# Kernel tuning notes

Measured on AMD Instinct MI355X. Metric: run time of the kernel, lower is better.

Reference implementation:

```python
import jax, jax.numpy as jnp
import numpy as np

INPUT_DIM = 1024
HIDDEN_DIM = 1024

def setup_inputs() -> dict:
    key = jax.random.key(0)
    ks = jax.random.split(key, 9)
    s_in = 1.0 / np.sqrt(INPUT_DIM)
    s_h = 1.0 / np.sqrt(HIDDEN_DIM)
    x = jax.random.normal(ks[0], (4, 2048, INPUT_DIM), dtype=jnp.float32)
    Wq = jax.random.uniform(ks[1], (INPUT_DIM, HIDDEN_DIM), jnp.float32, -s_in, s_in)
    bq = jax.random.uniform(ks[2], (HIDDEN_DIM,), jnp.float32, -s_in, s_in)
    Wk = jax.random.uniform(ks[3], (INPUT_DIM, HIDDEN_DIM), jnp.float32, -s_in, s_in)
    bk = jax.random.uniform(ks[4], (HIDDEN_DIM,), jnp.float32, -s_in, s_in)
    Wv = jax.random.uniform(ks[5], (INPUT_DIM, HIDDEN_DIM), jnp.float32, -s_in, s_in)
    bv = jax.random.uniform(ks[6], (HIDDEN_DIM,), jnp.float32, -s_in, s_in)
    Wo = jax.random.uniform(ks[7], (HIDDEN_DIM, INPUT_DIM), jnp.float32, -s_h, s_h)
    bo = jax.random.uniform(ks[8], (INPUT_DIM,), jnp.float32, -s_h, s_h)
    return {"x": x, "Wq": Wq, "bq": bq, "Wk": Wk, "bk": bk, "Wv": Wv, "bv": bv, "Wo": Wo, "bo": bo}

def reference(x, Wq, bq, Wk, bk, Wv, bv, Wo, bo):
    # x: [B, S, D_in]; scale uses x.shape[-1] (faithful to source, which divides by sqrt(input_dim))
    scale = 1.0 / jnp.sqrt(jnp.asarray(x.shape[-1], dtype=x.dtype))
    Q = jnp.einsum('bsd,dh->bsh', x, Wq) + bq
    K = jnp.einsum('bsd,dh->bsh', x, Wk) + bk
    V = jnp.einsum('bsd,dh->bsh', x, Wv) + bv
    scores = jnp.einsum('bqh,bkh->bqk', Q, K) * scale  # [B, S, S]
    attn = jax.nn.softmax(scores, axis=-1)
    ctx = jnp.einsum('bqk,bkh->bqh', attn, V)
    return jnp.einsum('bsh,hd->bsd', ctx, Wo) + bo
```

## Files before the change

kernel.cpp:

```cpp
#include <hip/hip_runtime.h>

typedef __attribute__((ext_vector_type(8))) short bf16x8;
typedef __attribute__((ext_vector_type(4))) float f32x4;
typedef __attribute__((ext_vector_type(4))) unsigned short us4;

#define AS1 __attribute__((address_space(1)))
#define AS3 __attribute__((address_space(3)))

__device__ __forceinline__ unsigned short f2bf(float f) {
  unsigned u = __float_as_uint(f);
  u += 0x7fff + ((u >> 16) & 1);
  return (unsigned short)(u >> 16);
}

__device__ __forceinline__ void gload_lds16(const void* g, void* l) {
  __builtin_amdgcn_global_load_lds((const AS1 unsigned int*)g,
                                   (AS3 unsigned int*)l, 16, 0, 0);
}

#define MFMA16(a, b, c) __builtin_amdgcn_mfma_f32_16x16x32_bf16(a, b, c, 0, 0, 0)

template <typename OutT, bool BIAS, int MODE>
__global__ __launch_bounds__(512, 2) void gemmk(
    const unsigned short* __restrict__ A,
    const unsigned short* __restrict__ Bt,
    OutT* __restrict__ C,
    unsigned short* __restrict__ Vt,
    const float* __restrict__ bias,
    int Kd, int lda, int ldb, int ldc,
    long sA, long sB, long sC,
    float scale) {
  constexpr int ABUF  = 256 * 32;
  constexpr int BUFSZ = ABUF + 128 * 32;
  __shared__ unsigned short lds[3 * BUFSZ];

  const int bz = blockIdx.z;
  A  += (size_t)bz * sA + (size_t)blockIdx.x * 256 * lda;
  Bt += (size_t)bz * sB + (size_t)blockIdx.y * 128 * ldb;

  const int tid  = threadIdx.x;
  const int wave = tid >> 6;
  const int lane = tid & 63;
  const int wm   = wave >> 1;
  const int wn   = wave & 1;
  const int l15  = lane & 15;
  const int hi   = lane >> 4;
  const int srow = tid >> 2;
  const int schk = (tid & 3) * 8;

  auto stage = [&](int bi, int k0) {
    unsigned short* L = &lds[bi * BUFSZ + wave * 512];
    const unsigned short* ga = A + (size_t)srow * lda + (k0 + schk);
    gload_lds16(ga, L);
    gload_lds16(ga + (size_t)128 * lda, L + 4096);
    gload_lds16(Bt + (size_t)srow * ldb + (k0 + schk), L + 8192);
  };

  f32x4 acc[4][4] = {};

  stage(0, 0);
  stage(1, 32);
  asm volatile("s_waitcnt vmcnt(3)" ::: "memory");
  __builtin_amdgcn_s_barrier();

  const int NT = Kd >> 5;
  int bufi = 0;
  const int rdA = (wm * 64 + l15) * 32 + hi * 8;
  const int rdB = ABUF + (wn * 64 + l15) * 32 + hi * 8;
  for (int t = 0; t < NT; ++t) {
    if (t + 2 < NT) {
      int nbi = bufi + 2; if (nbi >= 3) nbi -= 3;
      stage(nbi, (t + 2) << 5);
    }
    const unsigned short* L = &lds[bufi * BUFSZ];
    bf16x8 af[4], bf[4];
#pragma unroll
    for (int mt = 0; mt < 4; ++mt)
      af[mt] = *(const bf16x8*)&L[rdA + mt * 16 * 32];
#pragma unroll
    for (int nt = 0; nt < 4; ++nt)
      bf[nt] = *(const bf16x8*)&L[rdB + nt * 16 * 32];
    __builtin_amdgcn_s_setprio(1);
#pragma unroll
    for (int mt = 0; mt < 4; ++mt)
#pragma unroll
      for (int nt = 0; nt < 4; ++nt)
        acc[mt][nt] = MFMA16(af[mt], bf[nt], acc[mt][nt]);
    __builtin_amdgcn_s_setprio(0);
    if (t + 2 < NT)      asm volatile("s_waitcnt vmcnt(3)" ::: "memory");
    else if (t + 1 < NT) asm volatile("s_waitcnt vmcnt(0)" ::: "memory");
    __builtin_amdgcn_s_barrier();
    bufi = (bufi + 1 == 3) ? 0 : bufi + 1;
  }

  const int hi4  = hi << 2;
  const int row0 = blockIdx.x * 256 + wm * 64;
  const int col0 = blockIdx.y * 128 + wn * 64;

  if constexpr (MODE == 1) {
    const int piece = col0 >> 10;
    float bvv[4];
#pragma unroll
    for (int nt = 0; nt < 4; ++nt)
      bvv[nt] = BIAS ? bias[col0 + nt * 16 + l15] : 0.0f;
    if (piece < 2) {
      OutT* dst = C + (size_t)piece * sC;
      const int cb = (col0 & 1023) + l15;
#pragma unroll
      for (int mt = 0; mt < 4; ++mt)
#pragma unroll
        for (int r = 0; r < 4; ++r) {
          const size_t rowoff = (size_t)(row0 + mt * 16 + hi4 + r) * ldc;
#pragma unroll
          for (int nt = 0; nt < 4; ++nt)
            dst[rowoff + cb + nt * 16] = (OutT)f2bf(acc[mt][nt][r] * scale + bvv[nt]);
        }
    } else {
      const int b = blockIdx.x >> 3;
      const int sb = (blockIdx.x & 7) * 256 + wm * 64 + hi4;
#pragma unroll
      for (int nt = 0; nt < 4; ++nt) {
        const int d = ((col0 + nt * 16) & 1023) + l15;
#pragma unroll
        for (int mt = 0; mt < 4; ++mt) {
          us4 pk;
          pk.x = f2bf(acc[mt][nt][0] * scale + bvv[nt]);
          pk.y = f2bf(acc[mt][nt][1] * scale + bvv[nt]);
          pk.z = f2bf(acc[mt][nt][2] * scale + bvv[nt]);
          pk.w = f2bf(acc[mt][nt][3] * scale + bvv[nt]);
          *(us4*)&Vt[((size_t)b << 21) + (size_t)d * 2048 + sb + mt * 16] = pk;
        }
      }
    }
  } else {
    C += (size_t)bz * sC;
    float bvv[4];
#pragma unroll
    for (int nt = 0; nt < 4; ++nt)
      bvv[nt] = BIAS ? bias[col0 + nt * 16 + l15] : 0.0f;
    const int cb = col0 + l15;
#pragma unroll
    for (int mt = 0; mt < 4; ++mt)
#pragma unroll
      for (int r = 0; r < 4; ++r) {
        const size_t rowoff = (size_t)(row0 + mt * 16 + hi4 + r) * ldc;
#pragma unroll
        for (int nt = 0; nt < 4; ++nt) {
          const float v = acc[mt][nt][r] * scale + bvv[nt];
          if constexpr (sizeof(OutT) == 4)
            C[rowoff + cb + nt * 16] = v;
          else
            C[rowoff + cb + nt * 16] = (OutT)f2bf(v);
        }
      }
  }
}

__global__ void cvt_x(const float* __restrict__ in, unsigned short* __restrict__ out, int n4) {
  const int i = blockIdx.x * blockDim.x + threadIdx.x;
  if (i < n4) {
    const float4 v = ((const float4*)in)[i];
    uint2 o;
    o.x = (unsigned)f2bf(v.x) | ((unsigned)f2bf(v.y) << 16);
    o.y = (unsigned)f2bf(v.z) | ((unsigned)f2bf(v.w) << 16);
    ((uint2*)out)[i] = o;
  }
}

__global__ void cvtT_w4(const float* __restrict__ Wq, const float* __restrict__ Wk,
                        const float* __restrict__ Wv, const float* __restrict__ Wo,
                        unsigned short* __restrict__ Wqkvb, unsigned short* __restrict__ Wob) {
  __shared__ unsigned short tile[64][65];
  const int z = blockIdx.z;
  const float* in = (z == 0) ? Wq : (z == 1) ? Wk : (z == 2) ? Wv : Wo;
  unsigned short* out = (z == 3) ? Wob : Wqkvb + (size_t)z * 1024 * 1024;
  const int r0 = blockIdx.y * 64, c0 = blockIdx.x * 64;
  for (int i = threadIdx.y; i < 64; i += 4)
    tile[i][threadIdx.x] = f2bf(in[(size_t)(r0 + i) * 1024 + c0 + threadIdx.x]);
  __syncthreads();
  for (int i = threadIdx.y; i < 64; i += 4)
    out[(size_t)(c0 + i) * 1024 + r0 + threadIdx.x] = tile[threadIdx.x][i];
}

__global__ void concat_bias(const float* __restrict__ bq, const float* __restrict__ bk,
                            const float* __restrict__ bv, float* __restrict__ dst) {
  const int z = blockIdx.x;
  const float* src = (z == 0) ? bq : (z == 1) ? bk : bv;
  const int i = threadIdx.x;
  ((float4*)(dst + z * 1024))[i] = ((const float4*)src)[i];
}

__global__ __launch_bounds__(256) void softmax_bf16(unsigned short* __restrict__ scores) {
  unsigned short* p = scores + (size_t)blockIdx.x * 2048;
  const int t = threadIdx.x;
  uint4 raw = ((const uint4*)p)[t];
  float v[8];
  v[0] = __uint_as_float(raw.x << 16); v[1] = __uint_as_float(raw.x & 0xffff0000u);
  v[2] = __uint_as_float(raw.y << 16); v[3] = __uint_as_float(raw.y & 0xffff0000u);
  v[4] = __uint_as_float(raw.z << 16); v[5] = __uint_as_float(raw.z & 0xffff0000u);
  v[6] = __uint_as_float(raw.w << 16); v[7] = __uint_as_float(raw.w & 0xffff0000u);

  float m = v[0];
#pragma unroll
  for (int i = 1; i < 8; ++i) m = fmaxf(m, v[i]);
#pragma unroll
  for (int off = 32; off; off >>= 1) m = fmaxf(m, __shfl_xor(m, off, 64));

  __shared__ float red[4];
  __shared__ float bcast[2];
  const int wave = t >> 6, lane = t & 63;
  if (lane == 0) red[wave] = m;
  __syncthreads();
  if (t == 0) bcast[0] = fmaxf(fmaxf(red[0], red[1]), fmaxf(red[2], red[3]));
  __syncthreads();
  m = bcast[0];

  float s = 0.f;
#pragma unroll
  for (int i = 0; i < 8; ++i) { v[i] = __expf(v[i] - m); s += v[i]; }
#pragma unroll
  for (int off = 32; off; off >>= 1) s += __shfl_xor(s, off, 64);
  if (lane == 0) red[wave] = s;
  __syncthreads();
  if (t == 0) bcast[1] = red[0] + red[1] + red[2] + red[3];
  __syncthreads();
  const float inv = 1.0f / bcast[1];

  uint4 ov;
  ov.x = (unsigned)f2bf(v[0] * inv) | ((unsigned)f2bf(v[1] * inv) << 16);
  ov.y = (unsigned)f2bf(v[2] * inv) | ((unsigned)f2bf(v[3] * inv) << 16);
  ov.z = (unsigned)f2bf(v[4] * inv) | ((unsigned)f2bf(v[5] * inv) << 16);
  ov.w = (unsigned)f2bf(v[6] * inv) | ((unsigned)f2bf(v[7] * inv) << 16);
  ((uint4*)p)[t] = ov;
}

extern "C" void kernel_launch(void* const* d_in, const int* in_sizes, int n_in,
                              void* d_out, int out_size, void* d_ws, size_t ws_size,
                              hipStream_t stream) {
  const float* x  = (const float*)d_in[0];
  const float* Wq = (const float*)d_in[1];
  const float* bq = (const float*)d_in[2];
  const float* Wk = (const float*)d_in[3];
  const float* bk = (const float*)d_in[4];
  const float* Wv = (const float*)d_in[5];
  const float* bv = (const float*)d_in[6];
  const float* Wo = (const float*)d_in[7];
  const float* bo = (const float*)d_in[8];
  float* out = (float*)d_out;

  char* ws = (char*)d_ws;
  size_t off = 0;
  auto alloc = [&](size_t bytes) { char* p = ws + off; off += (bytes + 255) & ~255UL; return p; };
  unsigned short* xb    = (unsigned short*)alloc(8192UL * 1024 * 2);
  unsigned short* Wqkvb = (unsigned short*)alloc(3072UL * 1024 * 2);
  unsigned short* Wob   = (unsigned short*)alloc(1024UL * 1024 * 2);
  float*          bqkv  = (float*)alloc(3072UL * 4);
  unsigned short* Qb    = (unsigned short*)alloc(8192UL * 1024 * 2);
  unsigned short* Kb    = (unsigned short*)alloc(8192UL * 1024 * 2);
  unsigned short* Vtb   = (unsigned short*)alloc(4UL * 1024 * 2048 * 2);
  unsigned short* attn  = (unsigned short*)alloc(8192UL * 2048 * 2);
  unsigned short* ctxb  = (unsigned short*)alloc(8192UL * 1024 * 2);

  const dim3 blk(512);

  cvt_x<<<2097152 / 256, 256, 0, stream>>>(x, xb, 2097152);
  cvtT_w4<<<dim3(16, 16, 4), dim3(64, 4), 0, stream>>>(Wq, Wk, Wv, Wo, Wqkvb, Wob);
  concat_bias<<<3, 256, 0, stream>>>(bq, bk, bv, bqkv);

  gemmk<unsigned short, true, 1><<<dim3(32, 24, 1), blk, 0, stream>>>(
      xb, Wqkvb, Qb, Vtb, bqkv, 1024, 1024, 1024, 1024, 0, 0, 8192L * 1024, 1.0f);

  gemmk<unsigned short, false, 0><<<dim3(8, 16, 4), blk, 0, stream>>>(
      Qb, Kb, attn, nullptr, nullptr, 1024, 1024, 1024, 2048,
      2048L * 1024, 2048L * 1024, 2048L * 2048, 0.03125f);

  softmax_bf16<<<8192, 256, 0, stream>>>(attn);

  gemmk<unsigned short, false, 0><<<dim3(8, 8, 4), blk, 0, stream>>>(
      attn, Vtb, ctxb, nullptr, nullptr, 2048, 2048, 2048, 1024,
      2048L * 2048, 1024L * 2048, 2048L * 1024, 1.0f);

  gemmk<float, true, 0><<<dim3(32, 8, 1), blk, 0, stream>>>(
      ctxb, Wob, out, nullptr, bo, 1024, 1024, 1024, 1024, 0, 0, 0, 1.0f);
}
```

Before: 298.2 us.

## Template GEMM on N-tile width and use 256-wide tiles for QKV and scores

Makes the block N-tile width a template parameter and switches the QKV projection and QK^T score GEMMs to 256x256 tiles, so each block does twice the MFMA work per A-tile load. Each wave now owns 16 contiguous rows when staging into LDS, and fragments are read from contiguous 512-element chunks, which changes the LDS layout and is meant to reduce bank conflicts. The cost is double the accumulator registers (64 f32x4), larger LDS buffers and fewer blocks, which may lower occupancy below the 2-blocks launch bound and risk spills.

```diff
diff --git a/kernel.cpp b/kernel.cpp
--- a/kernel.cpp
+++ b/kernel.cpp
@@ -20,7 +20,7 @@
 
 #define MFMA16(a, b, c) __builtin_amdgcn_mfma_f32_16x16x32_bf16(a, b, c, 0, 0, 0)
 
-template <typename OutT, bool BIAS, int MODE>
+template <typename OutT, bool BIAS, int MODE, int BN>
 __global__ __launch_bounds__(512, 2) void gemmk(
     const unsigned short* __restrict__ A,
     const unsigned short* __restrict__ Bt,
@@ -30,13 +30,16 @@
     int Kd, int lda, int ldb, int ldc,
     long sA, long sB, long sC,
     float scale) {
-  constexpr int ABUF  = 256 * 32;
-  constexpr int BUFSZ = ABUF + 128 * 32;
+  constexpr int NB     = BN / 32;
+  constexpr int BCALLS = BN / 128;
+  constexpr int LOADS  = 2 + BCALLS;
+  constexpr int ABUF   = 256 * 32;
+  constexpr int BUFSZ  = ABUF + BN * 32;
   __shared__ unsigned short lds[3 * BUFSZ];
 
   const int bz = blockIdx.z;
   A  += (size_t)bz * sA + (size_t)blockIdx.x * 256 * lda;
-  Bt += (size_t)bz * sB + (size_t)blockIdx.y * 128 * ldb;
+  Bt += (size_t)bz * sB + (size_t)blockIdx.y * BN * ldb;
 
   const int tid  = threadIdx.x;
   const int wave = tid >> 6;
@@ -45,63 +48,70 @@
   const int wn   = wave & 1;
   const int l15  = lane & 15;
   const int hi   = lane >> 4;
-  const int srow = tid >> 2;
-  const int schk = (tid & 3) * 8;
+  const int srow = wave * 16 + l15;
+  const int scol = hi * 8;
 
   auto stage = [&](int bi, int k0) {
     unsigned short* L = &lds[bi * BUFSZ + wave * 512];
-    const unsigned short* ga = A + (size_t)srow * lda + (k0 + schk);
+    const unsigned short* ga = A + (size_t)srow * lda + (k0 + scol);
     gload_lds16(ga, L);
     gload_lds16(ga + (size_t)128 * lda, L + 4096);
-    gload_lds16(Bt + (size_t)srow * ldb + (k0 + schk), L + 8192);
+    const unsigned short* gb = Bt + (size_t)srow * ldb + (k0 + scol);
+    gload_lds16(gb, L + ABUF);
+    if constexpr (BCALLS == 2)
+      gload_lds16(gb + (size_t)128 * ldb, L + ABUF + 4096);
   };
 
-  f32x4 acc[4][4] = {};
+  f32x4 acc[4][NB] = {};
 
   stage(0, 0);
   stage(1, 32);
-  asm volatile("s_waitcnt vmcnt(3)" ::: "memory");
+  if constexpr (LOADS == 4) asm volatile("s_waitcnt vmcnt(4)" ::: "memory");
+  else                      asm volatile("s_waitcnt vmcnt(3)" ::: "memory");
   __builtin_amdgcn_s_barrier();
 
   const int NT = Kd >> 5;
   int bufi = 0;
-  const int rdA = (wm * 64 + l15) * 32 + hi * 8;
-  const int rdB = ABUF + (wn * 64 + l15) * 32 + hi * 8;
+  const int rdoff = lane * 8;
   for (int t = 0; t < NT; ++t) {
     if (t + 2 < NT) {
       int nbi = bufi + 2; if (nbi >= 3) nbi -= 3;
       stage(nbi, (t + 2) << 5);
     }
     const unsigned short* L = &lds[bufi * BUFSZ];
-    bf16x8 af[4], bf[4];
+    bf16x8 af[4], bf[NB];
 #pragma unroll
     for (int mt = 0; mt < 4; ++mt)
-      af[mt] = *(const bf16x8*)&L[rdA + mt * 16 * 32];
-#pragma unroll
-    for (int nt = 0; nt < 4; ++nt)
-      bf[nt] = *(const bf16x8*)&L[rdB + nt * 16 * 32];
+      af[mt] = *(const bf16x8*)&L[(wm * 4 + mt) * 512 + rdoff];
+#pragma unroll
+    for (int nt = 0; nt < NB; ++nt)
+      bf[nt] = *(const bf16x8*)&L[ABUF + (wn * NB + nt) * 512 + rdoff];
     __builtin_amdgcn_s_setprio(1);
 #pragma unroll
     for (int mt = 0; mt < 4; ++mt)
 #pragma unroll
-      for (int nt = 0; nt < 4; ++nt)
+      for (int nt = 0; nt < NB; ++nt)
         acc[mt][nt] = MFMA16(af[mt], bf[nt], acc[mt][nt]);
     __builtin_amdgcn_s_setprio(0);
-    if (t + 2 < NT)      asm volatile("s_waitcnt vmcnt(3)" ::: "memory");
-    else if (t + 1 < NT) asm volatile("s_waitcnt vmcnt(0)" ::: "memory");
+    if (t + 2 < NT) {
+      if constexpr (LOADS == 4) asm volatile("s_waitcnt vmcnt(4)" ::: "memory");
+      else                      asm volatile("s_waitcnt vmcnt(3)" ::: "memory");
+    } else if (t + 1 < NT) {
+      asm volatile("s_waitcnt vmcnt(0)" ::: "memory");
+    }
     __builtin_amdgcn_s_barrier();
     bufi = (bufi + 1 == 3) ? 0 : bufi + 1;
   }
 
   const int hi4  = hi << 2;
   const int row0 = blockIdx.x * 256 + wm * 64;
-  const int col0 = blockIdx.y * 128 + wn * 64;
+  const int col0 = blockIdx.y * BN + wn * (BN / 2);
 
   if constexpr (MODE == 1) {
     const int piece = col0 >> 10;
-    float bvv[4];
-#pragma unroll
-    for (int nt = 0; nt < 4; ++nt)
+    float bvv[NB];
+#pragma unroll
+    for (int nt = 0; nt < NB; ++nt)
       bvv[nt] = BIAS ? bias[col0 + nt * 16 + l15] : 0.0f;
     if (piece < 2) {
       OutT* dst = C + (size_t)piece * sC;
@@ -112,14 +122,14 @@
         for (int r = 0; r < 4; ++r) {
           const size_t rowoff = (size_t)(row0 + mt * 16 + hi4 + r) * ldc;
 #pragma unroll
-          for (int nt = 0; nt < 4; ++nt)
+          for (int nt = 0; nt < NB; ++nt)
             dst[rowoff + cb + nt * 16] = (OutT)f2bf(acc[mt][nt][r] * scale + bvv[nt]);
         }
     } else {
       const int b = blockIdx.x >> 3;
       const int sb = (blockIdx.x & 7) * 256 + wm * 64 + hi4;
 #pragma unroll
-      for (int nt = 0; nt < 4; ++nt) {
+      for (int nt = 0; nt < NB; ++nt) {
         const int d = ((col0 + nt * 16) & 1023) + l15;
 #pragma unroll
         for (int mt = 0; mt < 4; ++mt) {
@@ -134,9 +144,9 @@
     }
   } else {
     C += (size_t)bz * sC;
-    float bvv[4];
-#pragma unroll
-    for (int nt = 0; nt < 4; ++nt)
+    float bvv[NB];
+#pragma unroll
+    for (int nt = 0; nt < NB; ++nt)
       bvv[nt] = BIAS ? bias[col0 + nt * 16 + l15] : 0.0f;
     const int cb = col0 + l15;
 #pragma unroll
@@ -145,7 +155,7 @@
       for (int r = 0; r < 4; ++r) {
         const size_t rowoff = (size_t)(row0 + mt * 16 + hi4 + r) * ldc;
 #pragma unroll
-        for (int nt = 0; nt < 4; ++nt) {
+        for (int nt = 0; nt < NB; ++nt) {
           const float v = acc[mt][nt][r] * scale + bvv[nt];
           if constexpr (sizeof(OutT) == 4)
             C[rowoff + cb + nt * 16] = v;
@@ -267,19 +277,19 @@
   cvtT_w4<<<dim3(16, 16, 4), dim3(64, 4), 0, stream>>>(Wq, Wk, Wv, Wo, Wqkvb, Wob);
   concat_bias<<<3, 256, 0, stream>>>(bq, bk, bv, bqkv);
 
-  gemmk<unsigned short, true, 1><<<dim3(32, 24, 1), blk, 0, stream>>>(
+  gemmk<unsigned short, true, 1, 256><<<dim3(32, 12, 1), blk, 0, stream>>>(
       xb, Wqkvb, Qb, Vtb, bqkv, 1024, 1024, 1024, 1024, 0, 0, 8192L * 1024, 1.0f);
 
-  gemmk<unsigned short, false, 0><<<dim3(8, 16, 4), blk, 0, stream>>>(
+  gemmk<unsigned short, false, 0, 256><<<dim3(8, 8, 4), blk, 0, stream>>>(
       Qb, Kb, attn, nullptr, nullptr, 1024, 1024, 1024, 2048,
       2048L * 1024, 2048L * 1024, 2048L * 2048, 0.03125f);
 
   softmax_bf16<<<8192, 256, 0, stream>>>(attn);
 
-  gemmk<unsigned short, false, 0><<<dim3(8, 8, 4), blk, 0, stream>>>(
+  gemmk<unsigned short, false, 0, 128><<<dim3(8, 8, 4), blk, 0, stream>>>(
       attn, Vtb, ctxb, nullptr, nullptr, 2048, 2048, 2048, 1024,
       2048L * 2048, 1024L * 2048, 2048L * 1024, 1.0f);
 
-  gemmk<float, true, 0><<<dim3(32, 8, 1), blk, 0, stream>>>(
+  gemmk<float, true, 0, 128><<<dim3(32, 8, 1), blk, 0, stream>>>(
       ctxb, Wob, out, nullptr, bo, 1024, 1024, 1024, 1024, 0, 0, 0, 1.0f);
 }
```

Result: slower. 317.7 us (+6.5%).
